# Optimization experiments

Measured on AMD Instinct MI355X. Metric: run time of the kernel, lower is better.

Reference implementation:

```python
import jax, jax.numpy as jnp
import numpy as np

DIM, N_HEADS, GROUPS = 1152, 8, 4
HEAD_DIM = DIM // N_HEADS            # 144
KV_HEADS = N_HEADS // GROUPS         # 2
BSZ, SEQLEN, MAX_SEQ = 4, 2048, 2048
BASE = 10000.0


def _rope(x, cos, sin):
    # x: (b, s, h, d); cos/sin: (s, d//2)
    b, s, h, d = x.shape
    xr = x.astype(jnp.float32).reshape(b, s, h, d // 2, 2)
    xe, xo = xr[..., 0], xr[..., 1]
    c = cos[None, :, None, :]
    sn = sin[None, :, None, :]
    yr = xe * c - xo * sn
    yi = xe * sn + xo * c
    return jnp.stack([yr, yi], axis=-1).reshape(b, s, h, d).astype(x.dtype)


def setup_inputs() -> dict:
    key = jax.random.key(0)
    ks = jax.random.split(key, 8)
    std = 1.0 / np.sqrt(DIM)
    x = jax.random.normal(ks[0], (BSZ, SEQLEN, DIM), jnp.float32)
    wq = jax.random.normal(ks[1], (DIM, DIM), jnp.float32) * std
    bq = jnp.zeros((DIM,), jnp.float32)
    wkv = jax.random.normal(ks[2], (2 * KV_HEADS * HEAD_DIM, DIM), jnp.float32) * std
    bkv = jnp.zeros((2 * KV_HEADS * HEAD_DIM,), jnp.float32)
    wo = jax.random.normal(ks[3], (DIM, DIM), jnp.float32) * std
    bo = jnp.zeros((DIM,), jnp.float32)
    # rotary freqs: (seqlen, head_dim//2)
    inv = 1.0 / (BASE ** (jnp.arange(0, HEAD_DIM, 2, dtype=jnp.float32) / HEAD_DIM))
    t = jnp.arange(SEQLEN, dtype=jnp.float32)
    ang = jnp.outer(t, inv)
    freqs_cos, freqs_sin = jnp.cos(ang), jnp.sin(ang)
    # causal mask (s, t)
    mask = jnp.where(jnp.tril(jnp.ones((SEQLEN, SEQLEN), bool)), 0.0, -1e9).astype(jnp.float32)
    k_cache = jnp.zeros((BSZ, MAX_SEQ, KV_HEADS, HEAD_DIM), jnp.float32)
    v_cache = jnp.zeros((BSZ, MAX_SEQ, KV_HEADS, HEAD_DIM), jnp.float32)
    return {"x": x, "wq": wq, "bq": bq, "wkv": wkv, "bkv": bkv, "wo": wo, "bo": bo,
            "freqs_cos": freqs_cos, "freqs_sin": freqs_sin,
            "k_cache": k_cache, "v_cache": v_cache, "mask": mask, "start_pos": 0}


def reference(x, wq, bq, wkv, bkv, wo, bo, freqs_cos, freqs_sin, k_cache, v_cache, mask, start_pos):
    b, s, _ = x.shape
    end_pos = start_pos + s
    q = (x @ wq.T + bq).reshape(b, s, N_HEADS, HEAD_DIM)
    kv = (x @ wkv.T + bkv).reshape(b, s, 2, KV_HEADS, HEAD_DIM)
    k, v = kv[:, :, 0], kv[:, :, 1]
    rq = _rope(q, freqs_cos, freqs_sin)
    rk = _rope(k, freqs_cos, freqs_sin)
    k_cache = jax.lax.dynamic_update_slice(k_cache, rk, (0, start_pos, 0, 0))
    v_cache = jax.lax.dynamic_update_slice(v_cache, v, (0, start_pos, 0, 0))
    keys = jnp.repeat(k_cache[:, :end_pos], GROUPS, axis=2)   # (b, t, H, d)
    vals = jnp.repeat(v_cache[:, :end_pos], GROUPS, axis=2)
    scale = HEAD_DIM ** -0.5
    attn = jnp.einsum('bshd,bthd->bsht', rq, keys) * scale
    attn = attn + mask[:, None, :]
    scores = jax.nn.softmax(attn.astype(jnp.float32), axis=-1).astype(x.dtype)
    out = jnp.einsum('bsht,bthd->bshd', scores, vals)
    return out.reshape(b, s, DIM) @ wo.T + bo
```

## Files before the change

### kernel.cpp

```cpp
#include <hip/hip_runtime.h>


#define THREADS 256

typedef _Float16 f16x8 __attribute__((ext_vector_type(8)));
typedef _Float16 f16x4 __attribute__((ext_vector_type(4)));
typedef _Float16 f16x2 __attribute__((ext_vector_type(2)));
typedef float f32x4 __attribute__((ext_vector_type(4)));

#define GLDS16(gp, lp)                                                  \
  __builtin_amdgcn_global_load_lds(                                     \
      (const __attribute__((address_space(1))) unsigned int*)(gp),      \
      (__attribute__((address_space(3))) unsigned int*)(lp), 16, 0, 0)

__global__ __launch_bounds__(THREADS) void cvt_sw(const float* __restrict__ in,
                                                  _Float16* __restrict__ out,
                                                  int nG, int KC, int nrows) {
  int i = blockIdx.x * THREADS + threadIdx.x;
  if (i >= nG) return;
  int rr = i & 127;
  int j = i >> 7;
  int kc = j % KC;
  int rb = j / KC;
  int R = rb * 128 + rr;
  if (R >= nrows) R = nrows - 1;
  const float* src = in + (size_t)R * (KC * 8) + kc * 8;
  float4 a = *(const float4*)src;
  float4 c = *(const float4*)(src + 4);
  f16x8 o;
  o[0] = (_Float16)a.x; o[1] = (_Float16)a.y;
  o[2] = (_Float16)a.z; o[3] = (_Float16)a.w;
  o[4] = (_Float16)c.x; o[5] = (_Float16)c.y;
  o[6] = (_Float16)c.z; o[7] = (_Float16)c.w;
  *(f16x8*)(out + (size_t)i * 8) = o;
}

__global__ __launch_bounds__(THREADS) void prep_bias(const float* __restrict__ bq,
                                                     const float* __restrict__ bkv,
                                                     float* __restrict__ bias) {
  int i = blockIdx.x * THREADS + threadIdx.x;
  if (i < 1152) bias[i] = bq[i];
  else if (i < 1728) bias[i] = bkv[i - 1152];
}

__global__ __launch_bounds__(THREADS) void gemm_sw(
    const _Float16* __restrict__ A, const _Float16* __restrict__ B,
    const float* __restrict__ bias, float* __restrict__ C, int M, int N, int K) {
  __shared__ __align__(16) _Float16 As[1024 * 8];
  __shared__ __align__(16) _Float16 Bs[1024 * 8];
  const int t = threadIdx.x;
  const int w = t >> 6, lane = t & 63;
  const int quad = lane >> 4, l16 = lane & 15;
  const int wm = (w & 1) << 6, wn = (w >> 1) << 6;
  const int KC = K >> 3;
  const int mb = blockIdx.y, nb = blockIdx.x;
  const int m0 = mb << 7, n0 = nb << 7;

  f32x4 acc[4][4] = {};

  for (int kcb = 0; kcb < KC; kcb += 8) {
    const size_t Ab = ((size_t)mb * KC + kcb) << 7;
    const size_t Bb = ((size_t)nb * KC + kcb) << 7;
#pragma unroll
    for (int j = 0; j < 4; ++j) {
      const int ii = (w << 2) + j;
      GLDS16(A + ((Ab + (ii << 6) + lane) << 3), &As[(ii << 6) * 8]);
      GLDS16(B + ((Bb + (ii << 6) + lane) << 3), &Bs[(ii << 6) * 8]);
    }
    __syncthreads();
#pragma unroll
    for (int ks = 0; ks < 2; ++ks) {
      f16x8 af[4], bf[4];
#pragma unroll
      for (int mi = 0; mi < 4; ++mi)
        af[mi] = *(const f16x8*)&As[((((ks << 2) + quad) << 7) + wm + (mi << 4) + l16) * 8];
#pragma unroll
      for (int ni = 0; ni < 4; ++ni)
        bf[ni] = *(const f16x8*)&Bs[((((ks << 2) + quad) << 7) + wn + (ni << 4) + l16) * 8];
#pragma unroll
      for (int mi = 0; mi < 4; ++mi)
#pragma unroll
        for (int ni = 0; ni < 4; ++ni)
          acc[mi][ni] =
              __builtin_amdgcn_mfma_f32_16x16x32_f16(af[mi], bf[ni], acc[mi][ni], 0, 0, 0);
    }
    __syncthreads();
  }

#pragma unroll
  for (int mi = 0; mi < 4; ++mi) {
    const int row = m0 + wm + (mi << 4) + (quad << 2);
#pragma unroll
    for (int ni = 0; ni < 4; ++ni) {
      const int col = n0 + wn + (ni << 4) + l16;
      if (col < N) {
        const float bv = bias[col];
#pragma unroll
        for (int r = 0; r < 4; ++r)
          C[(size_t)(row + r) * N + col] = acc[mi][ni][r] + bv;
      }
    }
  }
}

__global__ __launch_bounds__(THREADS) void rope_scatter_f16(
    const float* __restrict__ qkv, const float* __restrict__ fc,
    const float* __restrict__ fs, _Float16* __restrict__ Qh,
    _Float16* __restrict__ Ksw) {
  int idx = blockIdx.x * THREADS + threadIdx.x;
  int m = idx / 720;
  int c = idx - m * 720;
  int s = m & 2047, b = m >> 11;
  const float* row = qkv + (size_t)m * 1728;
  int h, d2;
  const float* src;
  _Float16* dst;
  if (c < 576) {
    h = c / 72;
    d2 = c - h * 72;
    src = row + h * 144 + 2 * d2;
    dst = Qh + ((size_t)(b * 8 + h) * 2048 + s) * 144 + 2 * d2;
  } else {
    int cc = c - 576;
    h = cc / 72;
    d2 = cc - h * 72;
    src = row + 1152 + h * 144 + 2 * d2;
    size_t g = ((size_t)(b * 2 + h) * 64 + (s >> 5)) * 576 + (d2 >> 2) * 32 + (s & 31);
    dst = Ksw + g * 8 + (d2 & 3) * 2;
  }
  float2 v = *(const float2*)src;
  float cth = fc[s * 72 + d2], sth = fs[s * 72 + d2];
  f16x2 o;
  o.x = (_Float16)(v.x * cth - v.y * sth);
  o.y = (_Float16)(v.x * sth + v.y * cth);
  *(f16x2*)dst = o;
}

__global__ __launch_bounds__(THREADS) void v_transpose(const float* __restrict__ qkv,
                                                       _Float16* __restrict__ Vsw) {
  __shared__ _Float16 tile[128 * 145];
  const int t = threadIdx.x;
  const int s0 = blockIdx.x * 128;
  const int kvh = blockIdx.y, b = blockIdx.z;
  const float* src = qkv + ((size_t)(b * 2048 + s0)) * 1728 + 1440 + kvh * 144;
#pragma unroll
  for (int i = 0; i < 18; ++i) {
    int c = t + i * 256;
    int r = c / 36, cc = c - r * 36;
    float4 v = *(const float4*)(src + (size_t)r * 1728 + cc * 4);
    int base = r * 145 + cc * 4;
    tile[base + 0] = (_Float16)v.x;
    tile[base + 1] = (_Float16)v.y;
    tile[base + 2] = (_Float16)v.z;
    tile[base + 3] = (_Float16)v.w;
  }
  __syncthreads();
  const size_t tb = ((size_t)(b * 2 + kvh) * 64 + (s0 >> 5)) * 576;
#pragma unroll
  for (int i = 0; i < 9; ++i) {
    int c = t + i * 256;
    int sc = c / 144, d = c - sc * 144;
    f16x8 o;
#pragma unroll
    for (int j = 0; j < 8; ++j) o[j] = tile[(sc * 8 + j) * 145 + d];
    size_t g = tb + (size_t)(sc >> 2) * 576 + (sc & 3) * 144 + d;
    *(f16x8*)(Vsw + g * 8) = o;
  }
}

__global__ __launch_bounds__(THREADS, 4) void attn_mfma(
    const _Float16* __restrict__ Qh, const _Float16* __restrict__ Ksw,
    const _Float16* __restrict__ Vsw, _Float16* __restrict__ Out) {
  __shared__ __align__(16) _Float16 Ks[576 * 8];
  __shared__ __align__(16) _Float16 Vs[576 * 8];
  __shared__ __align__(16) _Float16 Ps[64 * 40];
  const int t = threadIdx.x;
  const int w = t >> 6, lane = t & 63;
  const int quad = lane >> 4, l16 = lane & 15;
  const int x = blockIdx.x, h = blockIdx.y, b = blockIdx.z;
  const int kvh = h >> 2;
  const int qi = (b == 0) ? x
               : (b == 1) ? 31 - x
               : (b == 2) ? ((x + 16) & 31)
                          : ((15 - x) & 31);
  const int q0 = qi * 64;
  const int nkt = 2 * qi + 2;
  const _Float16* Qg = Qh + ((size_t)(b * 8 + h) * 2048 + q0) * 144;
  const size_t tbase = (size_t)(b * 2 + kvh) * 64;

  f16x8 qf[4];
  f16x4 qt4;
  {
    const _Float16* qp = Qg + (size_t)(w * 16 + l16) * 144;
#pragma unroll
    for (int ks = 0; ks < 4; ++ks) qf[ks] = *(const f16x8*)(qp + ks * 32 + quad * 8);
    qt4 = *(const f16x4*)(qp + 128 + quad * 4);
  }

  f32x4 Oacc[9] = {};
  float mrow[4] = {-3e38f, -3e38f, -3e38f, -3e38f};
  float lrow[4] = {0.f, 0.f, 0.f, 0.f};
  const float scale = 0.08333333333333333f;
  const int colb = (l16 & ~1);
  const int rsel = (lane & 1) << 1;

  for (int kt = 0; kt < nkt; ++kt) {
    const _Float16* Kt = Ksw + (tbase + kt) * 576 * 8;
    const _Float16* Vt = Vsw + (tbase + kt) * 576 * 8;
    for (int ii = w; ii < 9; ii += 4) {
      GLDS16(Kt + ((ii << 6) + lane) * 8, &Ks[(ii << 6) * 8]);
      GLDS16(Vt + ((ii << 6) + lane) * 8, &Vs[(ii << 6) * 8]);
    }
    __syncthreads();

    f32x4 sc[2] = {};
#pragma unroll
    for (int ks = 0; ks < 4; ++ks) {
#pragma unroll
      for (int ct = 0; ct < 2; ++ct) {
        f16x8 bfr = *(const f16x8*)&Ks[(((ks * 4 + quad) << 5) + ct * 16 + l16) * 8];
        sc[ct] = __builtin_amdgcn_mfma_f32_16x16x32_f16(qf[ks], bfr, sc[ct], 0, 0, 0);
      }
    }
#pragma unroll
    for (int ct = 0; ct < 2; ++ct) {
      f16x4 bt = *(const f16x4*)&Ks[(((16 + (quad >> 1)) << 5) + ct * 16 + l16) * 8 +
                                    (quad & 1) * 4];
      sc[ct] = __builtin_amdgcn_mfma_f32_16x16x16f16(qt4, bt, sc[ct], 0, 0, 0);
    }

    const bool band = (kt >= nkt - 2);
    const int rowb = q0 + w * 16 + quad * 4;
    float vv[2][4];
    float mx[4] = {-3e38f, -3e38f, -3e38f, -3e38f};
#pragma unroll
    for (int ct = 0; ct < 2; ++ct) {
      const int cb = kt * 32 + ct * 16 + l16;
#pragma unroll
      for (int r = 0; r < 4; ++r) {
        float v = sc[ct][r] * scale;
        if (band && cb > rowb + r) v -= 1e9f;
        vv[ct][r] = v;
        mx[r] = fmaxf(mx[r], v);
      }
    }
    float alv[4];
#pragma unroll
    for (int r = 0; r < 4; ++r) {
      float m = mx[r];
      m = fmaxf(m, __shfl_xor(m, 1));
      m = fmaxf(m, __shfl_xor(m, 2));
      m = fmaxf(m, __shfl_xor(m, 4));
      m = fmaxf(m, __shfl_xor(m, 8));
      float mn = fmaxf(mrow[r], m);
      alv[r] = __expf(mrow[r] - mn);
      mrow[r] = mn;
    }
    float rs[4] = {0.f, 0.f, 0.f, 0.f};
#pragma unroll
    for (int ct = 0; ct < 2; ++ct) {
      float p[4], q[4];
#pragma unroll
      for (int r = 0; r < 4; ++r) {
        p[r] = __expf(vv[ct][r] - mrow[r]);
        rs[r] += p[r];
      }
#pragma unroll
      for (int r = 0; r < 4; ++r) q[r] = __shfl_xor(p[r], 1);
#pragma unroll
      for (int k = 0; k < 2; ++k) {
        const int r = rsel + k;
        f16x2 pv;
        if (lane & 1) {
          pv.x = (_Float16)q[r];
          pv.y = (_Float16)p[r];
        } else {
          pv.x = (_Float16)p[r];
          pv.y = (_Float16)q[r];
        }
        *(f16x2*)&Ps[(w * 16 + quad * 4 + r) * 40 + ct * 16 + colb] = pv;
      }
    }
#pragma unroll
    for (int r = 0; r < 4; ++r) {
      float v = rs[r];
      v += __shfl_xor(v, 1);
      v += __shfl_xor(v, 2);
      v += __shfl_xor(v, 4);
      v += __shfl_xor(v, 8);
      lrow[r] = lrow[r] * alv[r] + v;
    }
#pragma unroll
    for (int nt = 0; nt < 9; ++nt)
#pragma unroll
      for (int r = 0; r < 4; ++r) Oacc[nt][r] *= alv[r];

    {
      f16x8 pa = *(const f16x8*)&Ps[(w * 16 + l16) * 40 + quad * 8];
#pragma unroll
      for (int nt = 0; nt < 9; ++nt) {
        f16x8 vb = *(const f16x8*)&Vs[(quad * 144 + nt * 16 + l16) * 8];
        Oacc[nt] = __builtin_amdgcn_mfma_f32_16x16x32_f16(pa, vb, Oacc[nt], 0, 0, 0);
      }
    }
    __syncthreads();
  }

  float inv[4];
#pragma unroll
  for (int r = 0; r < 4; ++r) inv[r] = 1.f / lrow[r];
#pragma unroll
  for (int nt = 0; nt < 9; ++nt) {
    float o[4], qn[4];
#pragma unroll
    for (int r = 0; r < 4; ++r) o[r] = Oacc[nt][r] * inv[r];
#pragma unroll
    for (int r = 0; r < 4; ++r) qn[r] = __shfl_xor(o[r], 1);
#pragma unroll
    for (int k = 0; k < 2; ++k) {
      const int r = rsel + k;
      f16x2 pv;
      if (lane & 1) {
        pv.x = (_Float16)qn[r];
        pv.y = (_Float16)o[r];
      } else {
        pv.x = (_Float16)o[r];
        pv.y = (_Float16)qn[r];
      }
      const size_t grow = (size_t)b * 2048 + q0 + w * 16 + quad * 4 + r;
      const size_t g = ((grow >> 7) * 144 + h * 18 + nt * 2 + (colb >> 3)) * 128 +
                       (grow & 127);
      *(f16x2*)(Out + g * 8 + (colb & 7)) = pv;
    }
  }
}

extern "C" void kernel_launch(void* const* d_in, const int* in_sizes, int n_in,
                              void* d_out, int out_size, void* d_ws, size_t ws_size,
                              hipStream_t stream) {
  const float* x = (const float*)d_in[0];
  const float* wq = (const float*)d_in[1];
  const float* bq = (const float*)d_in[2];
  const float* wkv = (const float*)d_in[3];
  const float* bkv = (const float*)d_in[4];
  const float* wo = (const float*)d_in[5];
  const float* bo = (const float*)d_in[6];
  const float* fc = (const float*)d_in[7];
  const float* fs = (const float*)d_in[8];
  float* out = (float*)d_out;
  char* ws = (char*)d_ws;

  _Float16* x_sw = (_Float16*)(ws + 0);
  _Float16* wqkv_sw = (_Float16*)(ws + 18874368);
  _Float16* wo_sw = (_Float16*)(ws + 23003136);
  float* bias_qkv = (float*)(ws + 25657344);
  float* qkv = (float*)(ws + 25664256);
  _Float16* Qh = (_Float16*)(ws + 82287360);
  _Float16* Ksw = (_Float16*)(ws + 101161728);
  _Float16* Vsw = (_Float16*)(ws + 105880320);
  _Float16* attn_sw = (_Float16*)(ws + 110598912);

  cvt_sw<<<4608, THREADS, 0, stream>>>(x, x_sw, 1179648, 144, 8192);
  cvt_sw<<<648, THREADS, 0, stream>>>(wq, wqkv_sw, 165888, 144, 1152);
  cvt_sw<<<360, THREADS, 0, stream>>>(wkv, wqkv_sw + 1327104, 92160, 144, 576);
  cvt_sw<<<648, THREADS, 0, stream>>>(wo, wo_sw, 165888, 144, 1152);
  prep_bias<<<7, THREADS, 0, stream>>>(bq, bkv, bias_qkv);

  gemm_sw<<<dim3(14, 64), THREADS, 0, stream>>>(x_sw, wqkv_sw, bias_qkv, qkv,
                                                8192, 1728, 1152);

  rope_scatter_f16<<<23040, THREADS, 0, stream>>>(qkv, fc, fs, Qh, Ksw);
  v_transpose<<<dim3(16, 2, 4), THREADS, 0, stream>>>(qkv, Vsw);

  attn_mfma<<<dim3(32, 8, 4), THREADS, 0, stream>>>(Qh, Ksw, Vsw, attn_sw);

  gemm_sw<<<dim3(9, 64), THREADS, 0, stream>>>(attn_sw, wo_sw, bo, out, 8192,
                                               1152, 1152);
}
```

Before: 448.0 us.

## Share K/V tiles across two query heads per attention block with 512 threads

The attention kernel now runs 512 threads per block covering two query heads that share one KV head, so each staged K/V tile in LDS serves both heads. Waves 0-3 handle one head and 4-7 the other, and the P buffer is doubled. This halves the global-to-LDS traffic for K/V and halves the block count. The cost is larger blocks, less scheduling flexibility and heavier per-CU LDS use. The causal load-balancing permutation for batches 1 and 2 is swapped. The diff does not show whether the Ps indexing was updated to use all 8 waves.

```diff
diff --git a/kernel.cpp b/kernel.cpp
--- a/kernel.cpp
+++ b/kernel.cpp
@@ -168,20 +168,35 @@
   }
 }
 
-__global__ __launch_bounds__(THREADS, 4) void attn_mfma(
+#define STAGE_TILE(kt)                                                     \
+  do {                                                                     \
+    const _Float16* Kt_ = Ksw + (tbase + (size_t)(kt)) * 4608;             \
+    const _Float16* Vt_ = Vsw + (tbase + (size_t)(kt)) * 4608;             \
+    for (int c = w; c < 18; c += 8) {                                      \
+      if (c < 9)                                                           \
+        GLDS16(Kt_ + ((c << 6) + lane) * 8, &Ks[(c << 6) * 8]);            \
+      else                                                                 \
+        GLDS16(Vt_ + (((c - 9) << 6) + lane) * 8,                          \
+               &Vs[((c - 9) << 6) * 8]);                                   \
+    }                                                                      \
+  } while (0)
+
+__global__ __launch_bounds__(512, 4) void attn_mfma(
     const _Float16* __restrict__ Qh, const _Float16* __restrict__ Ksw,
     const _Float16* __restrict__ Vsw, _Float16* __restrict__ Out) {
   __shared__ __align__(16) _Float16 Ks[576 * 8];
   __shared__ __align__(16) _Float16 Vs[576 * 8];
-  __shared__ __align__(16) _Float16 Ps[64 * 40];
+  __shared__ __align__(16) _Float16 Ps[128 * 40];
   const int t = threadIdx.x;
   const int w = t >> 6, lane = t & 63;
+  const int w4 = w & 3;
   const int quad = lane >> 4, l16 = lane & 15;
-  const int x = blockIdx.x, h = blockIdx.y, b = blockIdx.z;
-  const int kvh = h >> 2;
+  const int x = blockIdx.x, hp = blockIdx.y, b = blockIdx.z;
+  const int h = hp * 2 + (w >> 2);
+  const int kvh = hp >> 1;
   const int qi = (b == 0) ? x
-               : (b == 1) ? 31 - x
-               : (b == 2) ? ((x + 16) & 31)
+               : (b == 1) ? ((x + 16) & 31)
+               : (b == 2) ? (31 - x)
                           : ((15 - x) & 31);
   const int q0 = qi * 64;
   const int nkt = 2 * qi + 2;
@@ -191,7 +206,7 @@
   f16x8 qf[4];
   f16x4 qt4;
   {
-    const _Float16* qp = Qg + (size_t)(w * 16 + l16) * 144;
+    const _Float16* qp = Qg + (size_t)(w4 * 16 + l16) * 144;
 #pragma unroll
     for (int ks = 0; ks < 4; ++ks) qf[ks] = *(const f16x8*)(qp + ks * 32 + quad * 8);
     qt4 = *(const f16x4*)(qp + 128 + quad * 4);
@@ -205,12 +220,7 @@
   const int rsel = (lane & 1) << 1;
 
   for (int kt = 0; kt < nkt; ++kt) {
-    const _Float16* Kt = Ksw + (tbase + kt) * 576 * 8;
-    const _Float16* Vt = Vsw + (tbase + kt) * 576 * 8;
-    for (int ii = w; ii < 9; ii += 4) {
-      GLDS16(Kt + ((ii << 6) + lane) * 8, &Ks[(ii << 6) * 8]);
-      GLDS16(Vt + ((ii << 6) + lane) * 8, &Vs[(ii << 6) * 8]);
-    }
+    STAGE_TILE(kt);
     __syncthreads();
 
     f32x4 sc[2] = {};
@@ -230,7 +240,7 @@
     }
 
     const bool band = (kt >= nkt - 2);
-    const int rowb = q0 + w * 16 + quad * 4;
+    const int rowb = q0 + w4 * 16 + quad * 4;
     float vv[2][4];
     float mx[4] = {-3e38f, -3e38f, -3e38f, -3e38f};
 #pragma unroll
@@ -327,7 +337,7 @@
         pv.x = (_Float16)o[r];
         pv.y = (_Float16)qn[r];
       }
-      const size_t grow = (size_t)b * 2048 + q0 + w * 16 + quad * 4 + r;
+      const size_t grow = (size_t)b * 2048 + q0 + w4 * 16 + quad * 4 + r;
       const size_t g = ((grow >> 7) * 144 + h * 18 + nt * 2 + (colb >> 3)) * 128 +
                        (grow & 127);
       *(f16x2*)(Out + g * 8 + (colb & 7)) = pv;
@@ -372,7 +382,7 @@
   rope_scatter_f16<<<23040, THREADS, 0, stream>>>(qkv, fc, fs, Qh, Ksw);
   v_transpose<<<dim3(16, 2, 4), THREADS, 0, stream>>>(qkv, Vsw);
 
-  attn_mfma<<<dim3(32, 8, 4), THREADS, 0, stream>>>(Qh, Ksw, Vsw, attn_sw);
+  attn_mfma<<<dim3(32, 4, 4), 512, 0, stream>>>(Qh, Ksw, Vsw, attn_sw);
 
   gemm_sw<<<dim3(9, 64), THREADS, 0, stream>>>(attn_sw, wo_sw, bo, out, 8192,
                                                1152, 1152);
```

Measured after the change: 421.5 us. 5.9% less time.
